# Kernel optimization log

Measured on AMD Instinct MI355X. Metric: run time of the kernel, lower is better.

Reference implementation:

```python
import jax, jax.numpy as jnp
import numpy as np

HEAD = 16
DIM = 1024
HEAD_DIM = DIM // HEAD


def setup_inputs() -> dict:
    key = jax.random.key(0)
    k1, k2, k3, k4 = jax.random.split(key, 4)
    x = jax.random.normal(k1, (2, 2048, DIM), dtype=jnp.float32)
    # nn.Linear(dim, 3*dim, bias=False): weight [3*dim, dim]
    w_qkv = jax.random.normal(k2, (3 * DIM, DIM), dtype=jnp.float32) * (DIM ** -0.5)
    # output proj nn.Linear(dim, dim)
    w_out = jax.random.normal(k3, (DIM, DIM), dtype=jnp.float32) * (DIM ** -0.5)
    b_out = jax.random.normal(k4, (DIM,), dtype=jnp.float32) * 0.01
    return {"x": x, "w_qkv": w_qkv, "w_out": w_out, "b_out": b_out}


def reference(x, w_qkv, w_out, b_out):
    b, s, _ = x.shape
    scale = HEAD_DIM ** -0.5
    qkv = jnp.einsum('bsd,ed->bse', x, w_qkv)  # [b, s, 3*dim]
    q, k, v = jnp.split(qkv, 3, axis=-1)
    def split_heads(t):
        return t.reshape(b, s, HEAD, HEAD_DIM).transpose(0, 2, 1, 3)  # b h s d
    q, k, v = split_heads(q), split_heads(k), split_heads(v)
    scores = jnp.einsum('bhqd,bhkd->bhqk', q, k) * scale
    attn = jax.nn.softmax(scores, axis=-1)
    out = jnp.einsum('bhqk,bhkd->bhqd', attn, v)
    out = out.transpose(0, 2, 1, 3).reshape(b, s, DIM)
    out = jnp.einsum('bsd,ed->bse', out, w_out) + b_out
    return out
```

## Files before the change

kernel.cpp:

```cpp
#include <hip/hip_runtime.h>
#include <hip/hip_bf16.h>
#include <stdint.h>

typedef __bf16 bf16_t;
typedef __attribute__((ext_vector_type(8))) __bf16 bf16x8;
typedef __attribute__((ext_vector_type(4))) __bf16 bf16x4v;
typedef __attribute__((ext_vector_type(4))) float f32x4;

#define GLOBAL_AS __attribute__((address_space(1)))
#define LDS_AS __attribute__((address_space(3)))

__device__ __forceinline__ void gload_lds16(const bf16_t* g, bf16_t* l) {
  __builtin_amdgcn_global_load_lds((const GLOBAL_AS void*)g, (LDS_AS void*)l, 16, 0, 0);
}

__device__ __forceinline__ uint32_t pk2(float a, float b) {
  union { bf16_t h[2]; uint32_t u; } x;
  x.h[0] = (bf16_t)a; x.h[1] = (bf16_t)b;
  return x.u;
}

__device__ __forceinline__ bf16x8 xpose8(bf16x8 v, int l) {
  union { bf16x8 v; uint32_t u[4]; } tv; tv.v = v;
  uint32_t a0 = __shfl_xor((int)tv.u[2], 4, 64);
  uint32_t a1 = __shfl_xor((int)tv.u[3], 4, 64);
  uint32_t a2 = __shfl_xor((int)tv.u[0], 4, 64);
  uint32_t a3 = __shfl_xor((int)tv.u[1], 4, 64);
  bool s4 = (l & 4) != 0;
  uint32_t n0 = s4 ? a0 : tv.u[0];
  uint32_t n1 = s4 ? a1 : tv.u[1];
  uint32_t n2 = s4 ? tv.u[2] : a2;
  uint32_t n3 = s4 ? tv.u[3] : a3;
  uint32_t b0 = __shfl_xor((int)n1, 2, 64);
  uint32_t b1 = __shfl_xor((int)n0, 2, 64);
  uint32_t b2 = __shfl_xor((int)n3, 2, 64);
  uint32_t b3 = __shfl_xor((int)n2, 2, 64);
  bool s2 = (l & 2) != 0;
  uint32_t m0 = s2 ? b0 : n0;
  uint32_t m1 = s2 ? n1 : b1;
  uint32_t m2 = s2 ? b2 : n2;
  uint32_t m3 = s2 ? n3 : b3;
  uint32_t c0 = __shfl_xor((int)m0, 1, 64);
  uint32_t c1 = __shfl_xor((int)m1, 1, 64);
  uint32_t c2 = __shfl_xor((int)m2, 1, 64);
  uint32_t c3 = __shfl_xor((int)m3, 1, 64);
  bool odd = (l & 1) != 0;
  union { uint32_t u[4]; bf16x8 v; } tw;
  tw.u[0] = odd ? ((m0 & 0xFFFF0000u) | (c0 >> 16)) : ((m0 & 0xFFFFu) | (c0 << 16));
  tw.u[1] = odd ? ((m1 & 0xFFFF0000u) | (c1 >> 16)) : ((m1 & 0xFFFFu) | (c1 << 16));
  tw.u[2] = odd ? ((m2 & 0xFFFF0000u) | (c2 >> 16)) : ((m2 & 0xFFFFu) | (c2 << 16));
  tw.u[3] = odd ? ((m3 & 0xFFFF0000u) | (c3 >> 16)) : ((m3 & 0xFFFFu) | (c3 << 16));
  return tw.v;
}

__global__ void cvt_f32_bf16(const float* __restrict__ in, bf16_t* __restrict__ out, int n) {
  int i = (blockIdx.x * 256 + threadIdx.x) * 4;
  if (i + 3 < n) {
    float4 v = *(const float4*)(in + i);
    bf16x4v o;
    o[0] = (bf16_t)v.x; o[1] = (bf16_t)v.y; o[2] = (bf16_t)v.z; o[3] = (bf16_t)v.w;
    *(bf16x4v*)(out + i) = o;
  }
}

template<int EPI>
__global__ __launch_bounds__(256)
void gemm_tn(const bf16_t* __restrict__ A, const bf16_t* __restrict__ B,
             void* __restrict__ Cout, const float* __restrict__ bias,
             int K, int ldc, int qcols, float qscale)
{
  __shared__ __align__(16) bf16_t As[128 * 32];
  __shared__ __align__(16) bf16_t Bs[128 * 32];
  const int t  = threadIdx.x;
  const int l  = t & 63, w = t >> 6;
  const int wm = w >> 1, wn = w & 1;
  const int lo = l & 15, hi = l >> 4;
  const int brow = blockIdx.y * 128;
  const int bcol = blockIdx.x * 128;

  const int i0 = t, i1 = t + 256;
  const int r0 = i0 >> 2, c0 = i0 & 3;
  const int r1 = i1 >> 2, c1 = i1 & 3;

  f32x4 acc[4][4] = {};

  for (int k0 = 0; k0 < K; k0 += 32) {
    gload_lds16(A + (size_t)(brow + r0) * K + k0 + c0 * 8, As + i0 * 8);
    gload_lds16(A + (size_t)(brow + r1) * K + k0 + c1 * 8, As + i1 * 8);
    gload_lds16(B + (size_t)(bcol + r0) * K + k0 + c0 * 8, Bs + i0 * 8);
    gload_lds16(B + (size_t)(bcol + r1) * K + k0 + c1 * 8, Bs + i1 * 8);
    __syncthreads();

    bf16x8 a[4], bb[4];
#pragma unroll
    for (int fm = 0; fm < 4; fm++)
      a[fm] = *(const bf16x8*)(As + (wm * 64 + fm * 16 + lo) * 32 + hi * 8);
#pragma unroll
    for (int fn = 0; fn < 4; fn++)
      bb[fn] = *(const bf16x8*)(Bs + (wn * 64 + fn * 16 + lo) * 32 + hi * 8);

#pragma unroll
    for (int fm = 0; fm < 4; fm++)
#pragma unroll
      for (int fn = 0; fn < 4; fn++)
        acc[fm][fn] = __builtin_amdgcn_mfma_f32_16x16x32_bf16(a[fm], bb[fn], acc[fm][fn], 0, 0, 0);
    __syncthreads();
  }

#pragma unroll
  for (int fm = 0; fm < 4; fm++) {
#pragma unroll
    for (int fn = 0; fn < 4; fn++) {
#pragma unroll
      for (int j = 0; j < 4; j++) {
        int row = brow + wm * 64 + fm * 16 + hi * 4 + j;
        int col = bcol + wn * 64 + fn * 16 + lo;
        float v = acc[fm][fn][j];
        if (EPI == 0) {
          if (col < qcols) v *= qscale;
          ((bf16_t*)Cout)[(size_t)row * ldc + col] = (bf16_t)v;
        } else {
          ((float*)Cout)[(size_t)row * ldc + col] = v + bias[col];
        }
      }
    }
  }
}

#define LDK 72

__global__ __launch_bounds__(256, 2)
void flash_attn(const bf16_t* __restrict__ qkv, bf16_t* __restrict__ aout)
{
  __shared__ __align__(16) bf16_t Kl[64 * LDK];
  __shared__ __align__(16) bf16_t Vt[64 * LDK];
  __shared__ __align__(16) bf16_t Pl[4][32 * LDK];

  const int t = threadIdx.x;
  const int l = t & 63, w = t >> 6;
  const int lo = l & 15, hi = l >> 4;
  int bid = (int)blockIdx.x;
  bid = (bid & 7) * 64 + (bid >> 3);
  const int qblk = bid & 15;
  const int bh   = bid >> 4;
  const int b = bh >> 4, h = bh & 15;
  const int rowbase = b * 2048;
  const int q0 = qblk * 128 + w * 32;

  const int r = l & 7, c = l >> 3;
  const int krow_w = w * 16 + r;
  const int vkey_w = 4 * w + (r >> 2) + 16 * (r & 3);
  const bf16_t* kvbase = qkv + (size_t)rowbase * 3072 + h * 64 + 1024;
  const size_t step = (size_t)64 * 3072;

  bf16x8 aq[2][2];
#pragma unroll
  for (int fm = 0; fm < 2; fm++)
#pragma unroll
    for (int kb = 0; kb < 2; kb++)
      aq[fm][kb] = *(const bf16x8*)(qkv + (size_t)(rowbase + q0 + fm * 16 + lo) * 3072
                                    + h * 64 + kb * 32 + hi * 8);

  bf16x8 ones;
#pragma unroll
  for (int j = 0; j < 8; j++) ones[j] = (bf16_t)1.0f;

  f32x4 oacc[2][4] = {};
  f32x4 ssum[2] = {};

  bf16x8 kch[2], vch[2];
#pragma unroll
  for (int i = 0; i < 2; i++) {
    kch[i] = *(const bf16x8*)(kvbase + (size_t)(krow_w + i * 8) * 3072 + c * 8);
    vch[i] = *(const bf16x8*)(kvbase + 1024 + (size_t)(vkey_w + 2 * i) * 3072 + c * 8);
  }

  bf16_t* plw = &Pl[w][0];
  const bf16_t* kv_next = kvbase + step;

  for (int it = 0; it < 32; ++it) {
    __syncthreads();
#pragma unroll
    for (int i = 0; i < 2; i++) {
      *(bf16x8*)(Kl + (krow_w + i * 8) * LDK + c * 8) = kch[i];
      bf16x8 tw = xpose8(vch[i], l);
      *(bf16x8*)(Vt + (c * 8 + r) * LDK + (w * 2 + i) * 8) = tw;
    }
    __syncthreads();

    if (it < 31) {
#pragma unroll
      for (int i = 0; i < 2; i++) {
        kch[i] = *(const bf16x8*)(kv_next + (size_t)(krow_w + i * 8) * 3072 + c * 8);
        vch[i] = *(const bf16x8*)(kv_next + 1024 + (size_t)(vkey_w + 2 * i) * 3072 + c * 8);
      }
      kv_next += step;
    }

    bf16x8 kf[4][2];
#pragma unroll
    for (int fn = 0; fn < 4; fn++)
#pragma unroll
      for (int kb = 0; kb < 2; kb++)
        kf[fn][kb] = *(const bf16x8*)(Kl + (fn * 16 + lo) * LDK + kb * 32 + hi * 8);
    f32x4 sacc[2][4] = {};
#pragma unroll
    for (int fm = 0; fm < 2; fm++)
#pragma unroll
      for (int fn = 0; fn < 4; fn++)
#pragma unroll
        for (int kb = 0; kb < 2; kb++)
          sacc[fm][fn] = __builtin_amdgcn_mfma_f32_16x16x32_bf16(aq[fm][kb], kf[fn][kb], sacc[fm][fn], 0, 0, 0);

#pragma unroll
    for (int fm = 0; fm < 2; fm++)
#pragma unroll
      for (int j = 0; j < 4; j++) {
        float p0 = __builtin_amdgcn_exp2f(sacc[fm][0][j]);
        float p1 = __builtin_amdgcn_exp2f(sacc[fm][1][j]);
        float p2 = __builtin_amdgcn_exp2f(sacc[fm][2][j]);
        float p3 = __builtin_amdgcn_exp2f(sacc[fm][3][j]);
        int row = fm * 16 + hi * 4 + j;
        uint2 d2; d2.x = pk2(p0, p1); d2.y = pk2(p2, p3);
        *(uint2*)(plw + row * LDK + lo * 4) = d2;
      }
    asm volatile("s_waitcnt lgkmcnt(0)" ::: "memory");
    __builtin_amdgcn_sched_barrier(0);

    bf16x8 pa[2][2], vb[4][2];
#pragma unroll
    for (int fm = 0; fm < 2; fm++)
#pragma unroll
      for (int kb = 0; kb < 2; kb++)
        pa[fm][kb] = *(const bf16x8*)(plw + (fm * 16 + lo) * LDK + kb * 32 + hi * 8);
#pragma unroll
    for (int fd = 0; fd < 4; fd++)
#pragma unroll
      for (int kb = 0; kb < 2; kb++)
        vb[fd][kb] = *(const bf16x8*)(Vt + (fd * 16 + lo) * LDK + kb * 32 + hi * 8);
#pragma unroll
    for (int fm = 0; fm < 2; fm++)
#pragma unroll
      for (int kb = 0; kb < 2; kb++)
        ssum[fm] = __builtin_amdgcn_mfma_f32_16x16x32_bf16(pa[fm][kb], ones, ssum[fm], 0, 0, 0);
#pragma unroll
    for (int fm = 0; fm < 2; fm++)
#pragma unroll
      for (int fd = 0; fd < 4; fd++)
#pragma unroll
        for (int kb = 0; kb < 2; kb++)
          oacc[fm][fd] = __builtin_amdgcn_mfma_f32_16x16x32_bf16(pa[fm][kb], vb[fd][kb], oacc[fm][fd], 0, 0, 0);
  }

#pragma unroll
  for (int fm = 0; fm < 2; fm++)
#pragma unroll
    for (int j = 0; j < 4; j++) {
      float inv = 1.0f / ssum[fm][j];
      int row = rowbase + q0 + fm * 16 + hi * 4 + j;
#pragma unroll
      for (int fd = 0; fd < 4; fd++) {
        int col = h * 64 + fd * 16 + lo;
        aout[(size_t)row * 1024 + col] = (bf16_t)(oacc[fm][fd][j] * inv);
      }
    }
}

extern "C" void kernel_launch(void* const* d_in, const int* in_sizes, int n_in,
                              void* d_out, int out_size, void* d_ws, size_t ws_size,
                              hipStream_t stream) {
  const float* x     = (const float*)d_in[0];
  const float* w_qkv = (const float*)d_in[1];
  const float* w_out = (const float*)d_in[2];
  const float* b_out = (const float*)d_in[3];

  char* ws = (char*)d_ws;
  bf16_t* xb   = (bf16_t*)(ws);
  bf16_t* wqb  = (bf16_t*)(ws + 8388608);
  bf16_t* wob  = (bf16_t*)(ws + 14680064);
  bf16_t* qkvb = (bf16_t*)(ws + 16777216);
  bf16_t* aob  = (bf16_t*)(ws + 41943040);

  cvt_f32_bf16<<<4096, 256, 0, stream>>>(x,     xb,  4194304);
  cvt_f32_bf16<<<3072, 256, 0, stream>>>(w_qkv, wqb, 3145728);
  cvt_f32_bf16<<<1024, 256, 0, stream>>>(w_out, wob, 1048576);

  dim3 g1(24, 32);
  gemm_tn<0><<<g1, 256, 0, stream>>>(xb, wqb, qkvb, nullptr, 1024, 3072, 1024, 0.18033688011f);

  flash_attn<<<512, 256, 0, stream>>>(qkvb, aob);

  dim3 g2(8, 32);
  gemm_tn<1><<<g2, 256, 0, stream>>>(aob, wob, d_out, b_out, 1024, 1024, 0, 1.0f);
}
```

Before: 146.8 us.

## Double-buffer K/V in LDS and keep P in registers via transposed QK MFMA

New measurement: 144.7 us. About the same (-1.4%).

```diff
diff --git a/kernel.cpp b/kernel.cpp
--- a/kernel.cpp
+++ b/kernel.cpp
@@ -132,9 +132,8 @@
 __global__ __launch_bounds__(256, 2)
 void flash_attn(const bf16_t* __restrict__ qkv, bf16_t* __restrict__ aout)
 {
-  __shared__ __align__(16) bf16_t Kl[64 * LDK];
-  __shared__ __align__(16) bf16_t Vt[64 * LDK];
-  __shared__ __align__(16) bf16_t Pl[4][32 * LDK];
+  __shared__ __align__(16) bf16_t Kl[2][64 * LDK];
+  __shared__ __align__(16) bf16_t Vt[2][64 * LDK];
 
   const int t = threadIdx.x;
   const int l = t & 63, w = t >> 6;
@@ -149,7 +148,7 @@
 
   const int r = l & 7, c = l >> 3;
   const int krow_w = w * 16 + r;
-  const int vkey_w = 4 * w + (r >> 2) + 16 * (r & 3);
+  const int vkey_w = 32 * (w >> 1) + 8 * (w & 1) + 16 * (r >> 2) + (r & 3);
   const bf16_t* kvbase = qkv + (size_t)rowbase * 3072 + h * 64 + 1024;
   const size_t step = (size_t)64 * 3072;
 
@@ -171,28 +170,42 @@
   bf16x8 kch[2], vch[2];
 #pragma unroll
   for (int i = 0; i < 2; i++) {
-    kch[i] = *(const bf16x8*)(kvbase + (size_t)(krow_w + i * 8) * 3072 + c * 8);
-    vch[i] = *(const bf16x8*)(kvbase + 1024 + (size_t)(vkey_w + 2 * i) * 3072 + c * 8);
-  }
-
-  bf16_t* plw = &Pl[w][0];
+    kch[i] = *(const bf16x8*)(kvbase + (size_t)(krow_w + 8 * i) * 3072 + c * 8);
+    vch[i] = *(const bf16x8*)(kvbase + 1024 + (size_t)(vkey_w + 4 * i) * 3072 + c * 8);
+  }
+#pragma unroll
+  for (int i = 0; i < 2; i++) {
+    *(bf16x8*)(&Kl[0][0] + (krow_w + 8 * i) * LDK + c * 8) = kch[i];
+    *(bf16x8*)(&Vt[0][0] + (c * 8 + r) * LDK + w * 16 + i * 8) = xpose8(vch[i], l);
+  }
   const bf16_t* kv_next = kvbase + step;
+#pragma unroll
+  for (int i = 0; i < 2; i++) {
+    kch[i] = *(const bf16x8*)(kv_next + (size_t)(krow_w + 8 * i) * 3072 + c * 8);
+    vch[i] = *(const bf16x8*)(kv_next + 1024 + (size_t)(vkey_w + 4 * i) * 3072 + c * 8);
+  }
+  kv_next += step;
 
   for (int it = 0; it < 32; ++it) {
     __syncthreads();
-#pragma unroll
-    for (int i = 0; i < 2; i++) {
-      *(bf16x8*)(Kl + (krow_w + i * 8) * LDK + c * 8) = kch[i];
-      bf16x8 tw = xpose8(vch[i], l);
-      *(bf16x8*)(Vt + (c * 8 + r) * LDK + (w * 2 + i) * 8) = tw;
-    }
-    __syncthreads();
+    const int cur = it & 1;
+    bf16_t* KlN = &Kl[cur ^ 1][0];
+    bf16_t* VtN = &Vt[cur ^ 1][0];
+    const bf16_t* KlC = &Kl[cur][0];
+    const bf16_t* VtC = &Vt[cur][0];
 
     if (it < 31) {
 #pragma unroll
       for (int i = 0; i < 2; i++) {
-        kch[i] = *(const bf16x8*)(kv_next + (size_t)(krow_w + i * 8) * 3072 + c * 8);
-        vch[i] = *(const bf16x8*)(kv_next + 1024 + (size_t)(vkey_w + 2 * i) * 3072 + c * 8);
+        *(bf16x8*)(KlN + (krow_w + 8 * i) * LDK + c * 8) = kch[i];
+        *(bf16x8*)(VtN + (c * 8 + r) * LDK + w * 16 + i * 8) = xpose8(vch[i], l);
+      }
+    }
+    if (it < 30) {
+#pragma unroll
+      for (int i = 0; i < 2; i++) {
+        kch[i] = *(const bf16x8*)(kv_next + (size_t)(krow_w + 8 * i) * 3072 + c * 8);
+        vch[i] = *(const bf16x8*)(kv_next + 1024 + (size_t)(vkey_w + 4 * i) * 3072 + c * 8);
       }
       kv_next += step;
     }
@@ -202,7 +215,7 @@
     for (int fn = 0; fn < 4; fn++)
 #pragma unroll
       for (int kb = 0; kb < 2; kb++)
-        kf[fn][kb] = *(const bf16x8*)(Kl + (fn * 16 + lo) * LDK + kb * 32 + hi * 8);
+        kf[fn][kb] = *(const bf16x8*)(KlC + (fn * 16 + lo) * LDK + kb * 32 + hi * 8);
     f32x4 sacc[2][4] = {};
 #pragma unroll
     for (int fm = 0; fm < 2; fm++)
@@ -210,34 +223,34 @@
       for (int fn = 0; fn < 4; fn++)
 #pragma unroll
         for (int kb = 0; kb < 2; kb++)
-          sacc[fm][fn] = __builtin_amdgcn_mfma_f32_16x16x32_bf16(aq[fm][kb], kf[fn][kb], sacc[fm][fn], 0, 0, 0);
-
-#pragma unroll
-    for (int fm = 0; fm < 2; fm++)
-#pragma unroll
-      for (int j = 0; j < 4; j++) {
-        float p0 = __builtin_amdgcn_exp2f(sacc[fm][0][j]);
-        float p1 = __builtin_amdgcn_exp2f(sacc[fm][1][j]);
-        float p2 = __builtin_amdgcn_exp2f(sacc[fm][2][j]);
-        float p3 = __builtin_amdgcn_exp2f(sacc[fm][3][j]);
-        int row = fm * 16 + hi * 4 + j;
-        uint2 d2; d2.x = pk2(p0, p1); d2.y = pk2(p2, p3);
-        *(uint2*)(plw + row * LDK + lo * 4) = d2;
-      }
-    asm volatile("s_waitcnt lgkmcnt(0)" ::: "memory");
-    __builtin_amdgcn_sched_barrier(0);
-
-    bf16x8 pa[2][2], vb[4][2];
-#pragma unroll
-    for (int fm = 0; fm < 2; fm++)
+          sacc[fm][fn] = __builtin_amdgcn_mfma_f32_16x16x32_bf16(kf[fn][kb], aq[fm][kb], sacc[fm][fn], 0, 0, 0);
+
+    bf16x8 pa[2][2];
+#pragma unroll
+    for (int fm = 0; fm < 2; fm++) {
+      float p[4][4];
+#pragma unroll
+      for (int fn = 0; fn < 4; fn++)
+#pragma unroll
+        for (int j = 0; j < 4; j++)
+          p[fn][j] = __builtin_amdgcn_exp2f(sacc[fm][fn][j]);
+#pragma unroll
+      for (int kb = 0; kb < 2; kb++) {
+        union { uint32_t u[4]; bf16x8 v; } pw;
+        pw.u[0] = pk2(p[2 * kb][0],     p[2 * kb][1]);
+        pw.u[1] = pk2(p[2 * kb][2],     p[2 * kb][3]);
+        pw.u[2] = pk2(p[2 * kb + 1][0], p[2 * kb + 1][1]);
+        pw.u[3] = pk2(p[2 * kb + 1][2], p[2 * kb + 1][3]);
+        pa[fm][kb] = pw.v;
+      }
+    }
+
+    bf16x8 vb[4][2];
+#pragma unroll
+    for (int fd = 0; fd < 4; fd++)
 #pragma unroll
       for (int kb = 0; kb < 2; kb++)
-        pa[fm][kb] = *(const bf16x8*)(plw + (fm * 16 + lo) * LDK + kb * 32 + hi * 8);
-#pragma unroll
-    for (int fd = 0; fd < 4; fd++)
-#pragma unroll
-      for (int kb = 0; kb < 2; kb++)
-        vb[fd][kb] = *(const bf16x8*)(Vt + (fd * 16 + lo) * LDK + kb * 32 + hi * 8);
+        vb[fd][kb] = *(const bf16x8*)(VtC + (fd * 16 + lo) * LDK + kb * 32 + hi * 8);
 #pragma unroll
     for (int fm = 0; fm < 2; fm++)
 #pragma unroll
```
